# Kernel tuning notes

Measured on AMD Instinct MI355X. Metric: run time of the kernel, lower is better.

## Reference

```python
import jax, jax.numpy as jnp
import numpy as np

B = 1024; PAST = 64; FUT = 16; N = PAST + FUT; DM = N // 3; HID = 64
EMB = [(2000, 32), (7, 8), (24, 8)]
OUTP = 3 + 32 + 8 + 8  # 51 = out_preprocess
O = OUTP - 1           # 50
HID1 = 64; HID2 = 64
NEG = -1e30  # finite stand-in for -inf so fully-masked rows stay NaN-free


def _gcnn(x, A, W, act):
    # D = diag((1 + rowsum(sign(relu(A-1e-15))))^-0.5); out = act(D @ A @ D @ (x W^T))
    d = (1.0 + (A > 1e-15).astype(x.dtype).sum(1)) ** -0.5
    An = d[:, None] * A * d[None, :]            # (P,P)
    h = jnp.einsum('pq,bqc->bpc', An, x @ W.T)  # (B,P,out)
    return jax.nn.relu(h) if act else h


def _forward(data, emb0, emb1, emb2, w1, b1, w2, b2, w3, b3,
             M, Wg1a, Wg1b, Wk, smoothing, Wg2a, Wg2b):
    # learned adjacency: masked softmax over strictly-lower-triangular support
    mask = jnp.tril(jnp.ones((N, N), data.dtype), -1)
    A0 = jax.nn.relu(M @ M.T)
    A = jax.nn.softmax(jnp.where(mask > 0, A0, NEG), axis=1)
    A = jnp.where(mask > 0, A, 0.0)
    # pre_processing: embeddings + MLP, then re-append last raw column
    tabs = (emb0, emb1, emb2)
    e = [t[data[:, :, i].astype(jnp.int32)] for i, t in enumerate(tabs)]
    h = jnp.concatenate(e + [data[:, :, -3:]], -1)        # (B,N,51)
    h = jax.nn.relu(h @ w1.T + b1)
    h = jax.nn.relu(h @ w2.T + b2)
    h = h @ w3.T + b3                                      # (B,N,50)
    x = jnp.concatenate([h, data[:, :, -1:]], -1)          # (B,N,51)
    sg1, sg2 = x[:, :PAST], x[:, PAST:]
    A11 = A[:PAST, :PAST]
    x1 = _gcnn(_gcnn(sg1, A11, Wg1a, True), A11, Wg1b, False)   # (B,PAST,50)
    xk = jnp.concatenate([x1, sg2[:, :, :-1]], 1)               # (B,N,50)
    y = x[:, :PAST, -1:]                                        # (B,PAST,1)
    # Kernel: batched Mahalanobis quadratic form (diagonal computed directly)
    xp, xf = xk[:, :PAST], xk[:, PAST:]
    theta = Wk @ Wk.T
    theta = (theta + theta.T) / 2
    diff = xp[:, None, :, :] - xf[:, :, None, :]                # (B,F,P,50)
    q = jnp.einsum('bjip,pq,bjiq->bji', diff, theta, diff)      # (B,F,P)
    alpha = -0.5 * q / (jax.nn.sigmoid(smoothing[0]) * 0.01)
    At = A[FUT:, :PAST] if False else A[PAST:, :PAST]           # (F,P)
    At = jax.nn.softmax(jnp.where(At != 0, At, NEG), axis=1)
    # torch Softmax(dim=1) on (B,F,P) normalizes over the F axis
    alpha = jax.nn.softmax(jnp.where(At[None] >= 0.004, alpha, NEG), axis=1)
    yh = jnp.einsum('bjp,bpo->bjo', alpha, y)                   # (B,F,1)
    x2 = jnp.concatenate([sg2[:, :, :-1], yh], -1)              # (B,F,51)
    A22 = A[PAST:, PAST:]
    out = _gcnn(_gcnn(x2, A22, Wg2a, True), A22, Wg2b, False).reshape(-1, FUT)
    # cdist(x, x), p=2, with NaN-safe sqrt at zero distance
    xc = jnp.concatenate([sg1, x2], 1)                          # (B,N,51)
    sq = jnp.sum(xc * xc, -1)
    d2 = jnp.maximum(sq[:, :, None] + sq[:, None, :]
                     - 2.0 * jnp.einsum('bnc,bmc->bnm', xc, xc), 0.0)
    dist = jnp.where(d2 > 0, jnp.sqrt(jnp.where(d2 > 0, d2, 1.0)), 0.0)
    return (out, dist, A)


def setup_inputs() -> dict:
    key = jax.random.key(0)
    ks = jax.random.split(key, 20)
    cols = [jax.random.randint(ks[i], (B, N, 1), 0, EMB[i][0]).astype(jnp.float32)
            for i in range(3)]
    data = jnp.concatenate(cols + [jax.random.normal(ks[3], (B, N, 3), jnp.float32)], -1)
    g = lambda k, s, sc: jax.random.normal(k, s, jnp.float32) * sc
    return dict(
        data=data,
        emb0=g(ks[4], EMB[0], 1.0),
        emb1=g(ks[5], EMB[1], 1.0),
        emb2=g(ks[6], EMB[2], 1.0),
        w1=g(ks[7], (128, OUTP), OUTP ** -0.5), b1=jnp.zeros((128,), jnp.float32),
        w2=g(ks[8], (128, 128), 128 ** -0.5), b2=jnp.zeros((128,), jnp.float32),
        w3=g(ks[9], (O, 128), 128 ** -0.5), b3=jnp.zeros((O,), jnp.float32),
        M=g(ks[10], (N, DM), 1.0),
        Wg1a=g(ks[11], (HID1, OUTP), OUTP ** -0.5),
        Wg1b=g(ks[12], (O, HID1), HID1 ** -0.5),
        Wk=g(ks[13], (O, HID), 0.05),
        smoothing=g(ks[14], (1,), 1.0),
        Wg2a=g(ks[15], (HID2, OUTP), OUTP ** -0.5),
        Wg2b=g(ks[16], (1, HID2), HID2 ** -0.5),
    )


def reference(data, emb0, emb1, emb2, w1, b1, w2, b2, w3, b3,
              M, Wg1a, Wg1b, Wk, smoothing, Wg2a, Wg2b):
    return _forward(data, emb0, emb1, emb2, w1, b1, w2, b2, w3, b3,
                    M, Wg1a, Wg1b, Wk, smoothing, Wg2a, Wg2b)
```

## Files before the change

### kernel.cpp

```cpp
#include <hip/hip_runtime.h>
#include <math.h>


#define NEGBIG (-1e30f)

#define OFF_X     0
#define OFF_X1    4177920
#define OFF_YH    7454720
#define OFF_A     7471104
#define OFF_AN22  7481600
#define OFF_MK    7484356
#define OFF_GAH   7514692
#define OFF_GAL   7516740
#define OFF_G2AT  7521156
#define OFF_SC    7524420
#define OFF_W1H   7524424
#define OFF_W1L   7528520
#define OFF_W2H   7532616
#define OFF_W2L   7540808
#define OFF_W3H   7549000
#define OFF_W3L   7553096
#define OFF_ANH   7557192
#define OFF_ANL   7559240
#define OFF_GBH   7561288
#define OFF_GBL   7563336
#define OFF_WKH   7565384
#define OFF_WKL   7567432

#define OUT_OUT   0
#define OUT_DIST  16384
#define OUT_A     6569984

typedef __attribute__((ext_vector_type(8))) short bf16x8;
typedef __attribute__((ext_vector_type(4))) short s16x4;
typedef __attribute__((ext_vector_type(4))) float f32x4;

__device__ __forceinline__ unsigned short f2bf(float x) {
  union { float f; unsigned u; } v; v.f = x;
  unsigned r = v.u + 0x7fffu + ((v.u >> 16) & 1u);
  return (unsigned short)(r >> 16);
}
__device__ __forceinline__ float bf2f(unsigned short h) {
  union { unsigned u; float f; } v; v.u = ((unsigned)h) << 16; return v.f;
}
__device__ __forceinline__ void split2(float v, unsigned short& h, unsigned short& l) {
  unsigned short hh = f2bf(v);
  h = hh;
  l = f2bf(v - bf2f(hh));
}
#define SWZ6(r, k) (((r) << 6) + (((((k) >> 3) ^ ((r) & 7)) << 3) | ((k) & 7)))
#define SWZ7(r, k) (((r) << 7) + (((((k) >> 3) ^ ((r) & 7)) << 3) | ((k) & 7)))

__global__ __launch_bounds__(256) void k_prep(
    const float* __restrict__ M, const float* __restrict__ Wk,
    const float* __restrict__ sm,
    const float* __restrict__ w1, const float* __restrict__ w2,
    const float* __restrict__ w3,
    const float* __restrict__ wg1a, const float* __restrict__ wg1b,
    const float* __restrict__ wg2a,
    float* __restrict__ ws, float* __restrict__ out)
{
  __shared__ float Msh[80 * 26];
  __shared__ float Ash[80 * 80];
  __shared__ float d1[64];
  __shared__ float d2s[16];
  const int t = threadIdx.x;

  if (blockIdx.x == 0) {
    for (int e = t; e < 80 * 26; e += 256) Msh[e] = M[e];
    __syncthreads();
    for (int e = t; e < 6400; e += 256) {
      int i = e / 80, j = e % 80;
      float v = 0.f;
      if (j < i) {
        float s = 0.f;
        for (int k = 0; k < 26; ++k) s += Msh[i * 26 + k] * Msh[j * 26 + k];
        v = s > 0.f ? s : 0.f;
      }
      Ash[e] = v;
    }
    __syncthreads();
    if (t > 0 && t < 80) {
      int i = t;
      float m = -3.4e38f;
      for (int j = 0; j < i; ++j) m = fmaxf(m, Ash[i * 80 + j]);
      float s = 0.f;
      for (int j = 0; j < i; ++j) {
        float e = expf(Ash[i * 80 + j] - m);
        Ash[i * 80 + j] = e;
        s += e;
      }
      float inv = 1.f / s;
      for (int j = 0; j < i; ++j) Ash[i * 80 + j] *= inv;
    }
    __syncthreads();
    {
      float* Aws = ws + OFF_A;
      float* Aout = out + OUT_A;
      for (int e = t; e < 6400; e += 256) { Aws[e] = Ash[e]; Aout[e] = Ash[e]; }
    }
    if (t < 64) {
      int c = 0;
      for (int j = 0; j < 64; ++j) if (Ash[t * 80 + j] > 1e-15f) ++c;
      d1[t] = 1.f / sqrtf(1.f + (float)c);
    } else if (t < 80) {
      int i = t - 64; int c = 0;
      for (int j = 0; j < 16; ++j) if (Ash[(64 + i) * 80 + 64 + j] > 1e-15f) ++c;
      d2s[i] = 1.f / sqrtf(1.f + (float)c);
    }
    __syncthreads();
    {
      float* an22 = ws + OFF_AN22;
      unsigned short* anH = (unsigned short*)(ws + OFF_ANH);
      unsigned short* anL = (unsigned short*)(ws + OFF_ANL);
      for (int e = t; e < 4096; e += 256) {
        int i = e >> 6, j = e & 63;
        float v = d1[i] * Ash[i * 80 + j] * d1[j];
        unsigned short h = f2bf(v);
        anH[e] = h; anL[e] = f2bf(v - bf2f(h));
      }
      for (int e = t; e < 256; e += 256) {
        int i = e >> 4, j = e & 15;
        an22[e] = d2s[i] * Ash[(64 + i) * 80 + 64 + j] * d2s[j];
      }
    }
    if (t < 16) {
      float* mk = ws + OFF_MK;
      int j = t;
      float m = -3.4e38f;
      for (int i = 0; i < 64; ++i) {
        float v = Ash[(64 + j) * 80 + i];
        v = (v != 0.f) ? v : NEGBIG;
        m = fmaxf(m, v);
      }
      float s = 0.f;
      for (int i = 0; i < 64; ++i) {
        float v = Ash[(64 + j) * 80 + i];
        v = (v != 0.f) ? v : NEGBIG;
        s += expf(v - m);
      }
      float inv = 1.f / s;
      for (int i = 0; i < 64; ++i) {
        float v = Ash[(64 + j) * 80 + i];
        v = (v != 0.f) ? v : NEGBIG;
        mk[j * 64 + i] = (expf(v - m) * inv >= 0.004f) ? 1.f : 0.f;
      }
    }
  } else if (blockIdx.x == 1) {
    unsigned short* wkh = (unsigned short*)(ws + OFF_WKH);
    unsigned short* wkl = (unsigned short*)(ws + OFF_WKL);
    for (int e = t; e < 4096; e += 256) {
      int h = e >> 6, o = e & 63;
      float v = (o < 50) ? Wk[o * 64 + h] : 0.f;
      unsigned short hh = f2bf(v);
      wkh[e] = hh; wkl[e] = f2bf(v - bf2f(hh));
    }
    if (t == 0) {
      float v = sm[0];
      float sig = 1.f / (1.f + expf(-v));
      (ws + OFF_SC)[0] = -0.5f / (sig * 0.01f);
    }
  } else if (blockIdx.x == 2) {
    unsigned short* w1h = (unsigned short*)(ws + OFF_W1H);
    unsigned short* w1l = (unsigned short*)(ws + OFF_W1L);
    for (int e = t; e < 8192; e += 256) {
      int n = e >> 6, k = e & 63;
      float v = (k < 51) ? w1[n * 51 + k] : 0.f;
      unsigned short h = f2bf(v);
      w1h[e] = h; w1l[e] = f2bf(v - bf2f(h));
    }
    unsigned short* w3h = (unsigned short*)(ws + OFF_W3H);
    unsigned short* w3l = (unsigned short*)(ws + OFF_W3L);
    for (int e = t; e < 8192; e += 256) {
      int n = e >> 7, k = e & 127;
      float v = (n < 50) ? w3[n * 128 + k] : 0.f;
      unsigned short h = f2bf(v);
      w3h[e] = h; w3l[e] = f2bf(v - bf2f(h));
    }
    unsigned short* gah = (unsigned short*)(ws + OFF_GAH);
    unsigned short* gal = (unsigned short*)(ws + OFF_GAL);
    for (int e = t; e < 4096; e += 256) {
      int n = e >> 6, k = e & 63;
      float v = (k < 51) ? wg1a[n * 51 + k] : 0.f;
      unsigned short h = f2bf(v);
      gah[e] = h; gal[e] = f2bf(v - bf2f(h));
    }
  } else {
    unsigned short* w2h = (unsigned short*)(ws + OFF_W2H);
    unsigned short* w2l = (unsigned short*)(ws + OFF_W2L);
    for (int e = t; e < 16384; e += 256) {
      int n = e >> 7, k = e & 127;
      float v = w2[n * 128 + k];
      unsigned short h = f2bf(v);
      w2h[e] = h; w2l[e] = f2bf(v - bf2f(h));
    }
    unsigned short* gbh = (unsigned short*)(ws + OFF_GBH);
    unsigned short* gbl = (unsigned short*)(ws + OFF_GBL);
    for (int e = t; e < 4096; e += 256) {
      int n = e >> 6, k = e & 63;
      float v = (n < 50) ? wg1b[n * 64 + k] : 0.f;
      unsigned short h = f2bf(v);
      gbh[e] = h; gbl[e] = f2bf(v - bf2f(h));
    }
    float* g2at = ws + OFF_G2AT;
    for (int e = t; e < 64 * 51; e += 256) { int o = e / 51, k = e % 51; g2at[k * 64 + o] = wg2a[e]; }
  }
}

__global__ __launch_bounds__(512) void k_mlp(
    const float* __restrict__ data,
    const float* __restrict__ emb0, const float* __restrict__ emb1,
    const float* __restrict__ emb2,
    const float* __restrict__ b1, const float* __restrict__ b2,
    const float* __restrict__ b3,
    float* __restrict__ ws)
{
  __shared__ __align__(16) unsigned short actH[64 * 128];
  __shared__ __align__(16) unsigned short actL[64 * 128];
  __shared__ __align__(16) unsigned short wbH[8192];
  __shared__ __align__(16) unsigned short wbL[8192];
  const int t = threadIdx.x;
  const int lane = t & 63, wave = t >> 6;
  const int s = wave & 3, half = wave >> 2;
  const int m16 = lane & 15, quad = lane >> 4;
  const int base = blockIdx.x * 64;
  const int row0 = s * 16;
  const int arow = row0 + m16;
  const unsigned short* w1h = (const unsigned short*)(ws + OFF_W1H);
  const unsigned short* w1l = (const unsigned short*)(ws + OFF_W1L);
  const unsigned short* w2h = (const unsigned short*)(ws + OFF_W2H);
  const unsigned short* w2l = (const unsigned short*)(ws + OFF_W2L);
  const unsigned short* w3h = (const unsigned short*)(ws + OFF_W3H);
  const unsigned short* w3l = (const unsigned short*)(ws + OFF_W3L);
  float* x = ws + OFF_X;

  for (int e = t; e < 4096; e += 512) {
    int r = e >> 6, c = e & 63;
    int g = base + r;
    float v = 0.f;
    if (c < 32)      { int i0 = (int)data[g * 6 + 0]; v = emb0[i0 * 32 + c]; }
    else if (c < 40) { int i1 = (int)data[g * 6 + 1]; v = emb1[i1 * 8 + (c - 32)]; }
    else if (c < 48) { int i2 = (int)data[g * 6 + 2]; v = emb2[i2 * 8 + (c - 40)]; }
    else if (c < 51) { v = data[g * 6 + 3 + (c - 48)]; }
    int idx = SWZ7(r, c);
    split2(v, actH[idx], actL[idx]);
  }
  for (int q = t; q < 1024; q += 512) {
    int col = q >> 3, c = q & 7;
    int dst = (col << 6) + ((c ^ (col & 7)) << 3);
    *(bf16x8*)(wbH + dst) = *(const bf16x8*)(w1h + (col << 6) + (c << 3));
    *(bf16x8*)(wbL + dst) = *(const bf16x8*)(w1l + (col << 6) + (c << 3));
  }
  __syncthreads();

  {
    f32x4 acc[4];
#pragma unroll
    for (int n = 0; n < 4; ++n) acc[n] = (f32x4){0.f, 0.f, 0.f, 0.f};
#pragma unroll
    for (int kb8 = 0; kb8 < 8; kb8 += 4) {
      int ach = ((quad + kb8) ^ (m16 & 7)) << 3;
      bf16x8 aH = *(const bf16x8*)(actH + (arow << 7) + ach);
      bf16x8 aL = *(const bf16x8*)(actL + (arow << 7) + ach);
#pragma unroll
      for (int n = 0; n < 4; ++n) {
        const int col = (half * 4 + n) * 16 + m16;
        int boff = (col << 6) + ach;
        bf16x8 bH = *(const bf16x8*)(wbH + boff);
        bf16x8 bL = *(const bf16x8*)(wbL + boff);
        acc[n] = __builtin_amdgcn_mfma_f32_16x16x32_bf16(aH, bH, acc[n], 0, 0, 0);
        acc[n] = __builtin_amdgcn_mfma_f32_16x16x32_bf16(aH, bL, acc[n], 0, 0, 0);
        acc[n] = __builtin_amdgcn_mfma_f32_16x16x32_bf16(aL, bH, acc[n], 0, 0, 0);
      }
    }
#pragma unroll
    for (int n = 0; n < 4; ++n) {
      const int col = (half * 4 + n) * 16 + m16;
      const float bias = b1[col];
#pragma unroll
      for (int r = 0; r < 4; ++r) {
        float v = acc[n][r] + bias; v = v > 0.f ? v : 0.f;
        int idx = SWZ7(row0 + quad * 4 + r, col);
        split2(v, actH[idx], actL[idx]);
      }
    }
  }

  f32x4 acc2[2][2];
#pragma unroll
  for (int a2 = 0; a2 < 2; ++a2)
#pragma unroll
    for (int n = 0; n < 2; ++n) acc2[a2][n] = (f32x4){0.f, 0.f, 0.f, 0.f};
  for (int h2 = 0; h2 < 2; ++h2) {
    __syncthreads();
    for (int q = t; q < 1024; q += 512) {
      int coll = q >> 4, c = q & 15;
      int srcc = (((h2 << 6) + coll) << 7) + (c << 3);
      int dst = (coll << 7) + ((c ^ (coll & 7)) << 3);
      *(bf16x8*)(wbH + dst) = *(const bf16x8*)(w2h + srcc);
      *(bf16x8*)(wbL + dst) = *(const bf16x8*)(w2l + srcc);
    }
    __syncthreads();
#pragma unroll
    for (int kb8 = 0; kb8 < 16; kb8 += 4) {
      int ach = ((quad + kb8) ^ (m16 & 7)) << 3;
      bf16x8 aH = *(const bf16x8*)(actH + (arow << 7) + ach);
      bf16x8 aL = *(const bf16x8*)(actL + (arow << 7) + ach);
#pragma unroll
      for (int n = 0; n < 2; ++n) {
        const int cl = (half * 2 + n) * 16 + m16;
        int boff = (cl << 7) + ach;
        bf16x8 bH = *(const bf16x8*)(wbH + boff);
        bf16x8 bL = *(const bf16x8*)(wbL + boff);
        f32x4 a = acc2[h2][n];
        a = __builtin_amdgcn_mfma_f32_16x16x32_bf16(aH, bH, a, 0, 0, 0);
        a = __builtin_amdgcn_mfma_f32_16x16x32_bf16(aH, bL, a, 0, 0, 0);
        a = __builtin_amdgcn_mfma_f32_16x16x32_bf16(aL, bH, a, 0, 0, 0);
        acc2[h2][n] = a;
      }
    }
  }
  __syncthreads();
#pragma unroll
  for (int hh = 0; hh < 2; ++hh) {
#pragma unroll
    for (int n = 0; n < 2; ++n) {
      const int col = hh * 64 + (half * 2 + n) * 16 + m16;
      const float bias = b2[col];
#pragma unroll
      for (int r = 0; r < 4; ++r) {
        float v = acc2[hh][n][r] + bias; v = v > 0.f ? v : 0.f;
        int idx = SWZ7(row0 + quad * 4 + r, col);
        split2(v, actH[idx], actL[idx]);
      }
    }
  }

  for (int q = t; q < 1024; q += 512) {
    int coll = q >> 4, c = q & 15;
    int dst = (coll << 7) + ((c ^ (coll & 7)) << 3);
    *(bf16x8*)(wbH + dst) = *(const bf16x8*)(w3h + (coll << 7) + (c << 3));
    *(bf16x8*)(wbL + dst) = *(const bf16x8*)(w3l + (coll << 7) + (c << 3));
  }
  __syncthreads();
  {
    f32x4 acc[2];
#pragma unroll
    for (int n = 0; n < 2; ++n) acc[n] = (f32x4){0.f, 0.f, 0.f, 0.f};
#pragma unroll
    for (int kb8 = 0; kb8 < 16; kb8 += 4) {
      int ach = ((quad + kb8) ^ (m16 & 7)) << 3;
      bf16x8 aH = *(const bf16x8*)(actH + (arow << 7) + ach);
      bf16x8 aL = *(const bf16x8*)(actL + (arow << 7) + ach);
#pragma unroll
      for (int n = 0; n < 2; ++n) {
        const int col = (half * 2 + n) * 16 + m16;
        int boff = (col << 7) + ach;
        bf16x8 bH = *(const bf16x8*)(wbH + boff);
        bf16x8 bL = *(const bf16x8*)(wbL + boff);
        acc[n] = __builtin_amdgcn_mfma_f32_16x16x32_bf16(aH, bH, acc[n], 0, 0, 0);
        acc[n] = __builtin_amdgcn_mfma_f32_16x16x32_bf16(aH, bL, acc[n], 0, 0, 0);
        acc[n] = __builtin_amdgcn_mfma_f32_16x16x32_bf16(aL, bH, acc[n], 0, 0, 0);
      }
    }
#pragma unroll
    for (int n = 0; n < 2; ++n) {
      const int col = (half * 2 + n) * 16 + m16;
      if (col < 50) {
        const float bias = b3[col];
#pragma unroll
        for (int r = 0; r < 4; ++r) {
          int row = row0 + quad * 4 + r;
          x[(base + row) * 51 + col] = acc[n][r] + bias;
        }
      }
    }
  }
  if (t < 64) x[(base + t) * 51 + 50] = data[(base + t) * 6 + 5];
}

__global__ __launch_bounds__(512) void k_g1(float* __restrict__ ws)
{
  __shared__ __align__(16) unsigned short b1H[4096], b1L[4096];
  __shared__ __align__(16) unsigned short b2H[4096], b2L[4096];
  __shared__ __align__(16) unsigned short anH[4096], anL[4096];
  __shared__ __align__(16) unsigned short wH[4096],  wL[4096];
  const int t = threadIdx.x, b = blockIdx.x;
  const int lane = t & 63, wave = t >> 6;
  const int s = wave & 3, half = wave >> 2;
  const int m16 = lane & 15, quad = lane >> 4;
  const int row0 = s * 16;
  const int arow = row0 + m16;
  const float* x = ws + OFF_X;
  const unsigned short* gAnH = (const unsigned short*)(ws + OFF_ANH);
  const unsigned short* gAnL = (const unsigned short*)(ws + OFF_ANL);
  const unsigned short* gaH = (const unsigned short*)(ws + OFF_GAH);
  const unsigned short* gaL = (const unsigned short*)(ws + OFF_GAL);
  const unsigned short* gbH = (const unsigned short*)(ws + OFF_GBH);
  const unsigned short* gbL = (const unsigned short*)(ws + OFF_GBL);
  float* x1 = ws + OFF_X1;

  for (int e = t; e < 4096; e += 512) {
    int r = e >> 6, k = e & 63;
    float v = (k < 51) ? x[(b * 80 + r) * 51 + k] : 0.f;
    int idx = SWZ6(r, k);
    split2(v, b1H[idx], b1L[idx]);
  }
  for (int q = t; q < 512; q += 512) {
    int r = q >> 3, c = q & 7;
    int dst = (r << 6) + ((c ^ (r & 7)) << 3);
    int src = (r << 6) + (c << 3);
    *(bf16x8*)(anH + dst) = *(const bf16x8*)(gAnH + src);
    *(bf16x8*)(anL + dst) = *(const bf16x8*)(gAnL + src);
    *(bf16x8*)(wH + dst)  = *(const bf16x8*)(gaH + src);
    *(bf16x8*)(wL + dst)  = *(const bf16x8*)(gaL + src);
  }
  __syncthreads();

  {
    f32x4 acc[2];
#pragma unroll
    for (int n = 0; n < 2; ++n) acc[n] = (f32x4){0.f, 0.f, 0.f, 0.f};
#pragma unroll
    for (int kb8 = 0; kb8 < 8; kb8 += 4) {
      int ach = ((quad + kb8) ^ (m16 & 7)) << 3;
      bf16x8 aH = *(const bf16x8*)(b1H + (arow << 6) + ach);
      bf16x8 aL = *(const bf16x8*)(b1L + (arow << 6) + ach);
#pragma unroll
      for (int n = 0; n < 2; ++n) {
        const int col = (half * 2 + n) * 16 + m16;
        int boff = (col << 6) + ach;
        bf16x8 bH = *(const bf16x8*)(wH + boff);
        bf16x8 bL = *(const bf16x8*)(wL + boff);
        acc[n] = __builtin_amdgcn_mfma_f32_16x16x32_bf16(aH, bH, acc[n], 0, 0, 0);
        acc[n] = __builtin_amdgcn_mfma_f32_16x16x32_bf16(aH, bL, acc[n], 0, 0, 0);
        acc[n] = __builtin_amdgcn_mfma_f32_16x16x32_bf16(aL, bH, acc[n], 0, 0, 0);
      }
    }
    const int kb = row0 + quad * 4;
#pragma unroll
    for (int n = 0; n < 2; ++n) {
      const int col = (half * 2 + n) * 16 + m16;
      int idx = (col << 6) + (((((kb >> 3) ^ (col & 7)) << 3)) | (kb & 7));
      s16x4 hv, lv;
#pragma unroll
      for (int r = 0; r < 4; ++r) {
        unsigned short hh, ll; split2(acc[n][r], hh, ll);
        hv[r] = (short)hh; lv[r] = (short)ll;
      }
      *(s16x4*)(b2H + idx) = hv; *(s16x4*)(b2L + idx) = lv;
    }
  }
  __syncthreads();

  for (int q = t; q < 512; q += 512) {
    int r = q >> 3, c = q & 7;
    int dst = (r << 6) + ((c ^ (r & 7)) << 3);
    int src = (r << 6) + (c << 3);
    *(bf16x8*)(wH + dst) = *(const bf16x8*)(gbH + src);
    *(bf16x8*)(wL + dst) = *(const bf16x8*)(gbL + src);
  }
  f32x4 accP[2];
  {
#pragma unroll
    for (int n = 0; n < 2; ++n) accP[n] = (f32x4){0.f, 0.f, 0.f, 0.f};
#pragma unroll
    for (int kb8 = 0; kb8 < 8; kb8 += 4) {
      int ach = ((quad + kb8) ^ (m16 & 7)) << 3;
      bf16x8 aH = *(const bf16x8*)(anH + (arow << 6) + ach);
      bf16x8 aL = *(const bf16x8*)(anL + (arow << 6) + ach);
#pragma unroll
      for (int n = 0; n < 2; ++n) {
        const int col = (half * 2 + n) * 16 + m16;
        int boff = (col << 6) + ach;
        bf16x8 bH = *(const bf16x8*)(b2H + boff);
        bf16x8 bL = *(const bf16x8*)(b2L + boff);
        accP[n] = __builtin_amdgcn_mfma_f32_16x16x32_bf16(aH, bH, accP[n], 0, 0, 0);
        accP[n] = __builtin_amdgcn_mfma_f32_16x16x32_bf16(aH, bL, accP[n], 0, 0, 0);
        accP[n] = __builtin_amdgcn_mfma_f32_16x16x32_bf16(aL, bH, accP[n], 0, 0, 0);
      }
    }
  }
  __syncthreads();
  {
    const int kb = row0 + quad * 4;
#pragma unroll
    for (int n = 0; n < 2; ++n) {
      const int col = (half * 2 + n) * 16 + m16;
      int idx = (col << 6) + (((((kb >> 3) ^ (col & 7)) << 3)) | (kb & 7));
      s16x4 hv, lv;
#pragma unroll
      for (int r = 0; r < 4; ++r) {
        float v = accP[n][r]; v = v > 0.f ? v : 0.f;
        unsigned short hh, ll; split2(v, hh, ll);
        hv[r] = (short)hh; lv[r] = (short)ll;
      }
      *(s16x4*)(b2H + idx) = hv; *(s16x4*)(b2L + idx) = lv;
    }
  }
  __syncthreads();

  {
    f32x4 acc[2];
#pragma unroll
    for (int n = 0; n < 2; ++n) acc[n] = (f32x4){0.f, 0.f, 0.f, 0.f};
#pragma unroll
    for (int kb8 = 0; kb8 < 8; kb8 += 4) {
      int ach = ((quad + kb8) ^ (m16 & 7)) << 3;
      bf16x8 aH = *(const bf16x8*)(anH + (arow << 6) + ach);
      bf16x8 aL = *(const bf16x8*)(anL + (arow << 6) + ach);
#pragma unroll
      for (int n = 0; n < 2; ++n) {
        const int col = (half * 2 + n) * 16 + m16;
        int boff = (col << 6) + ach;
        bf16x8 bH = *(const bf16x8*)(b2H + boff);
        bf16x8 bL = *(const bf16x8*)(b2L + boff);
        acc[n] = __builtin_amdgcn_mfma_f32_16x16x32_bf16(aH, bH, acc[n], 0, 0, 0);
        acc[n] = __builtin_amdgcn_mfma_f32_16x16x32_bf16(aH, bL, acc[n], 0, 0, 0);
        acc[n] = __builtin_amdgcn_mfma_f32_16x16x32_bf16(aL, bH, acc[n], 0, 0, 0);
      }
    }
#pragma unroll
    for (int n = 0; n < 2; ++n) {
      const int col = (half * 2 + n) * 16 + m16;
#pragma unroll
      for (int r = 0; r < 4; ++r) {
        int idx = SWZ6(row0 + quad * 4 + r, col);
        split2(acc[n][r], b1H[idx], b1L[idx]);
      }
    }
  }
  __syncthreads();

  {
    f32x4 acc[2];
#pragma unroll
    for (int n = 0; n < 2; ++n) acc[n] = (f32x4){0.f, 0.f, 0.f, 0.f};
#pragma unroll
    for (int kb8 = 0; kb8 < 8; kb8 += 4) {
      int ach = ((quad + kb8) ^ (m16 & 7)) << 3;
      bf16x8 aH = *(const bf16x8*)(b1H + (arow << 6) + ach);
      bf16x8 aL = *(const bf16x8*)(b1L + (arow << 6) + ach);
#pragma unroll
      for (int n = 0; n < 2; ++n) {
        const int col = (half * 2 + n) * 16 + m16;
        int boff = (col << 6) + ach;
        bf16x8 bH = *(const bf16x8*)(wH + boff);
        bf16x8 bL = *(const bf16x8*)(wL + boff);
        acc[n] = __builtin_amdgcn_mfma_f32_16x16x32_bf16(aH, bH, acc[n], 0, 0, 0);
        acc[n] = __builtin_amdgcn_mfma_f32_16x16x32_bf16(aH, bL, acc[n], 0, 0, 0);
        acc[n] = __builtin_amdgcn_mfma_f32_16x16x32_bf16(aL, bH, acc[n], 0, 0, 0);
      }
    }
#pragma unroll
    for (int n = 0; n < 2; ++n) {
      const int col = (half * 2 + n) * 16 + m16;
      if (col < 50) {
#pragma unroll
        for (int r = 0; r < 4; ++r) {
          int row = row0 + quad * 4 + r;
          x1[(b * 64 + row) * 50 + col] = acc[n][r];
        }
      }
    }
  }
}

__global__ __launch_bounds__(512) void k_q(const float* __restrict__ wg2b,
                                           float* __restrict__ ws,
                                           float* __restrict__ out)
{
  __shared__ __align__(16) unsigned short zH[4096], zL[4096];
  __shared__ __align__(16) unsigned char bufB[16384];
  __shared__ __align__(16) unsigned short xfH[1024], xfL[1024];
  __shared__ __align__(16) unsigned short zfH[1024], zfL[1024];
  __shared__ float spal[64 * 34];
  __shared__ float sp[64], sf[16], yv[64], yhs[16];
  const int t = threadIdx.x, b = blockIdx.x;
  const int lane = t & 63, wave = t >> 6;
  const int s = wave & 3, half = wave >> 2;
  const int m16 = lane & 15, quad = lane >> 4;
  const int row0 = s * 16;
  const int arow = row0 + m16;
  const float* x = ws + OFF_X;
  const float* x1 = ws + OFF_X1;
  const float* mk = ws + OFF_MK;
  const float* an22 = ws + OFF_AN22;
  const float* g2at = ws + OFF_G2AT;
  const float sc = (ws + OFF_SC)[0];
  float* yh = ws + OFF_YH;

  unsigned short* wkH = (unsigned short*)bufB;
  unsigned short* wkL = wkH + 4096;

  for (int e = t; e < 4096; e += 512) {
    int r = e >> 6, c = e & 63;
    float v = (c < 50) ? x1[(b * 64 + r) * 50 + c] : 0.f;
    int idx = SWZ6(r, c);
    split2(v, zH[idx], zL[idx]);
  }
  for (int e = t; e < 1024; e += 512) {
    int r = e >> 6, c = e & 63;
    float v = (c < 50) ? x[(b * 80 + 64 + r) * 51 + c] : 0.f;
    int idx = SWZ6(r, c);
    split2(v, xfH[idx], xfL[idx]);
  }
  {
    const unsigned short* gwkH = (const unsigned short*)(ws + OFF_WKH);
    const unsigned short* gwkL = (const unsigned short*)(ws + OFF_WKL);
    for (int q = t; q < 512; q += 512) {
      int r = q >> 3, c = q & 7;
      int dst = (r << 6) + ((c ^ (r & 7)) << 3);
      int src = (r << 6) + (c << 3);
      *(bf16x8*)(wkH + dst) = *(const bf16x8*)(gwkH + src);
      *(bf16x8*)(wkL + dst) = *(const bf16x8*)(gwkL + src);
    }
  }
  if (t < 64) yv[t] = x[(b * 80 + t) * 51 + 50];
  __syncthreads();

  f32x4 accZ[2];
#pragma unroll
  for (int n = 0; n < 2; ++n) accZ[n] = (f32x4){0.f, 0.f, 0.f, 0.f};
#pragma unroll
  for (int kb8 = 0; kb8 < 8; kb8 += 4) {
    int ach = ((quad + kb8) ^ (m16 & 7)) << 3;
    bf16x8 aH = *(const bf16x8*)(zH + (arow << 6) + ach);
    bf16x8 aL = *(const bf16x8*)(zL + (arow << 6) + ach);
#pragma unroll
    for (int n = 0; n < 2; ++n) {
      const int col = (half * 2 + n) * 16 + m16;
      int boff = (col << 6) + ach;
      bf16x8 bH = *(const bf16x8*)(wkH + boff);
      bf16x8 bL = *(const bf16x8*)(wkL + boff);
      accZ[n] = __builtin_amdgcn_mfma_f32_16x16x32_bf16(aH, bH, accZ[n], 0, 0, 0);
      accZ[n] = __builtin_amdgcn_mfma_f32_16x16x32_bf16(aH, bL, accZ[n], 0, 0, 0);
      accZ[n] = __builtin_amdgcn_mfma_f32_16x16x32_bf16(aL, bH, accZ[n], 0, 0, 0);
      accZ[n] = __builtin_amdgcn_mfma_f32_16x16x32_bf16(aL, bL, accZ[n], 0, 0, 0);
    }
  }
  if (half == 0) {
    f32x4 af = (f32x4){0.f, 0.f, 0.f, 0.f};
#pragma unroll
    for (int kb8 = 0; kb8 < 8; kb8 += 4) {
      int ach = ((quad + kb8) ^ (m16 & 7)) << 3;
      bf16x8 aH = *(const bf16x8*)(xfH + (m16 << 6) + ach);
      bf16x8 aL = *(const bf16x8*)(xfL + (m16 << 6) + ach);
      const int col = s * 16 + m16;
      int boff = (col << 6) + ach;
      bf16x8 bH = *(const bf16x8*)(wkH + boff);
      bf16x8 bL = *(const bf16x8*)(wkL + boff);
      af = __builtin_amdgcn_mfma_f32_16x16x32_bf16(aH, bH, af, 0, 0, 0);
      af = __builtin_amdgcn_mfma_f32_16x16x32_bf16(aH, bL, af, 0, 0, 0);
      af = __builtin_amdgcn_mfma_f32_16x16x32_bf16(aL, bH, af, 0, 0, 0);
      af = __builtin_amdgcn_mfma_f32_16x16x32_bf16(aL, bL, af, 0, 0, 0);
    }
    const int h = s * 16 + m16;
#pragma unroll
    for (int r = 0; r < 4; ++r) {
      int idx = SWZ6(quad * 4 + r, h);
      split2(af[r], zfH[idx], zfL[idx]);
    }
  }
  __syncthreads();

  {
    float s2[4] = {0.f, 0.f, 0.f, 0.f};
#pragma unroll
    for (int n = 0; n < 2; ++n) {
      const int h = (half * 2 + n) * 16 + m16;
#pragma unroll
      for (int r = 0; r < 4; ++r) {
        float v = accZ[n][r];
        s2[r] += v * v;
        int idx = SWZ6(row0 + quad * 4 + r, h);
        split2(v, zH[idx], zL[idx]);
      }
    }
#pragma unroll
    for (int r = 0; r < 4; ++r)
      spal[(row0 + quad * 4 + r) * 34 + half * 16 + m16] = s2[r];
  }
  __syncthreads();

  if (t < 64) {
    float ssum = 0.f;
#pragma unroll
    for (int m = 0; m < 32; ++m) ssum += spal[t * 34 + m];
    sp[t] = ssum;
  } else if (t < 80) {
    int j = t - 64;
    float ssum = 0.f;
    for (int h = 0; h < 64; ++h) {
      int idx = SWZ6(j, h);
      float v = bf2f(zfH[idx]) + bf2f(zfL[idx]);
      ssum += v * v;
    }
    sf[j] = ssum;
  }
  __syncthreads();

  {
    f32x4 ac2 = (f32x4){0.f, 0.f, 0.f, 0.f};
#pragma unroll
    for (int kb8 = 0; kb8 < 8; kb8 += 4) {
      int ach = ((quad + kb8) ^ (m16 & 7)) << 3;
      bf16x8 aH = *(const bf16x8*)(zH + (arow << 6) + ach);
      bf16x8 aL = *(const bf16x8*)(zL + (arow << 6) + ach);
      bf16x8 bH = *(const bf16x8*)(zfH + (m16 << 6) + ach);
      bf16x8 bL = *(const bf16x8*)(zfL + (m16 << 6) + ach);
      ac2 = __builtin_amdgcn_mfma_f32_16x16x32_bf16(aH, bH, ac2, 0, 0, 0);
      ac2 = __builtin_amdgcn_mfma_f32_16x16x32_bf16(aH, bL, ac2, 0, 0, 0);
      ac2 = __builtin_amdgcn_mfma_f32_16x16x32_bf16(aL, bH, ac2, 0, 0, 0);
      ac2 = __builtin_amdgcn_mfma_f32_16x16x32_bf16(aL, bL, ac2, 0, 0, 0);
    }
    if (half == 0) {
      float* al = spal;
#pragma unroll
      for (int r = 0; r < 4; ++r) {
        int i = row0 + quad * 4 + r;
        al[i * 17 + m16] = sc * (sp[i] + sf[m16] - 2.f * ac2[r]);
      }
    }
  }
  __syncthreads();
  {
    float* al = spal;
    if (t < 64) {
      const int i = t;
      float lv[16];
      float m = -3.4e38f;
#pragma unroll
      for (int j = 0; j < 16; ++j) {
        float v = (mk[j * 64 + i] != 0.f) ? al[i * 17 + j] : NEGBIG;
        lv[j] = v;
        m = fmaxf(m, v);
      }
      float ssum = 0.f;
#pragma unroll
      for (int j = 0; j < 16; ++j) { lv[j] = expf(lv[j] - m); ssum += lv[j]; }
      float inv = 1.f / ssum;
#pragma unroll
      for (int j = 0; j < 16; ++j) al[i * 17 + j] = lv[j] * inv;
    }
  }
  __syncthreads();
  if (t < 16) {
    float* al = spal;
    float ssum = 0.f;
    for (int i = 0; i < 64; ++i) ssum += al[i * 17 + t] * yv[i];
    yh[b * 16 + t] = ssum;
    yhs[t] = ssum;
  }
  __syncthreads();

  float* X2  = (float*)bufB;
  float* A22 = X2 + 832;
  float* G   = A22 + 256;
  float* Pm  = G + 1024;
  float* wb  = Pm + 1024;
  float* zz  = wb + 64;

  for (int e = t; e < 832; e += 512) {
    int r = e / 52, c = e - r * 52;
    float v = 0.f;
    if (c < 50)       v = x[(b * 80 + 64 + r) * 51 + c];
    else if (c == 50) v = yhs[r];
    X2[e] = v;
  }
  for (int e = t; e < 256; e += 512) A22[e] = an22[e];
  if (t < 64) wb[t] = wg2b[t];
  __syncthreads();
  for (int e = t; e < 1024; e += 512) {
    int j = e >> 6, h = e & 63;
    float ssum = 0.f;
    for (int k = 0; k < 51; ++k) ssum += X2[j * 52 + k] * g2at[k * 64 + h];
    G[e] = ssum;
  }
  __syncthreads();
  for (int e = t; e < 1024; e += 512) {
    int j = e >> 6, h = e & 63;
    float ssum = 0.f;
#pragma unroll
    for (int k = 0; k < 16; ++k) ssum += A22[j * 16 + k] * G[k * 64 + h];
    Pm[e] = ssum > 0.f ? ssum : 0.f;
  }
  __syncthreads();
  if (t < 16) {
    float ssum = 0.f;
    for (int h = 0; h < 64; ++h) ssum += Pm[t * 64 + h] * wb[h];
    zz[t] = ssum;
  }
  __syncthreads();
  if (t < 16) {
    float ssum = 0.f;
#pragma unroll
    for (int k = 0; k < 16; ++k) ssum += A22[t * 16 + k] * zz[k];
    out[OUT_OUT + b * 16 + t] = ssum;
  }
}

__global__ __launch_bounds__(320) void k_dist(float* __restrict__ ws,
                                              float* __restrict__ out)
{
  __shared__ __align__(16) unsigned short xcH[5120], xcL[5120];
  __shared__ float sq[80];
  const int t = threadIdx.x, b = blockIdx.x;
  const int lane = t & 63, wave = t >> 6;
  const int m16 = lane & 15, quad = lane >> 4;
  const int row0 = wave * 16;
  const int arow = row0 + m16;
  const float* x = ws + OFF_X;
  const float* yhg = ws + OFF_YH;
  float* dist = out + OUT_DIST + b * 6400;

  for (int e = t; e < 5120; e += 320) {
    int n = e >> 6, c = e & 63;
    float v = 0.f;
    if (c < 50)       v = x[(b * 80 + n) * 51 + c];
    else if (c == 50) v = (n < 64) ? x[(b * 80 + n) * 51 + 50] : yhg[b * 16 + (n - 64)];
    int idx = SWZ6(n, c);
    split2(v, xcH[idx], xcL[idx]);
  }
  __syncthreads();

  f32x4 acc[5];
#pragma unroll
  for (int n = 0; n < 5; ++n) acc[n] = (f32x4){0.f, 0.f, 0.f, 0.f};
#pragma unroll
  for (int kb8 = 0; kb8 < 8; kb8 += 4) {
    int ach = ((quad + kb8) ^ (m16 & 7)) << 3;
    bf16x8 aH = *(const bf16x8*)(xcH + (arow << 6) + ach);
    bf16x8 aL = *(const bf16x8*)(xcL + (arow << 6) + ach);
#pragma unroll
    for (int nf = 0; nf < 5; ++nf) {
      const int col = nf * 16 + m16;
      int boff = (col << 6) + ach;
      bf16x8 bH = *(const bf16x8*)(xcH + boff);
      bf16x8 bL = *(const bf16x8*)(xcL + boff);
      acc[nf] = __builtin_amdgcn_mfma_f32_16x16x32_bf16(aH, bH, acc[nf], 0, 0, 0);
      acc[nf] = __builtin_amdgcn_mfma_f32_16x16x32_bf16(aH, bL, acc[nf], 0, 0, 0);
      acc[nf] = __builtin_amdgcn_mfma_f32_16x16x32_bf16(aL, bH, acc[nf], 0, 0, 0);
    }
  }
  if ((m16 >> 2) == quad) sq[row0 + m16] = acc[wave][m16 & 3];
  __syncthreads();

#pragma unroll
  for (int nf = 0; nf < 5; ++nf) {
    const int m = nf * 16 + m16;
#pragma unroll
    for (int r = 0; r < 4; ++r) {
      int i = row0 + quad * 4 + r;
      float d2 = sq[i] + sq[m] - 2.f * acc[nf][r];
      d2 = d2 > 0.f ? d2 : 0.f;
      dist[i * 80 + m] = d2 > 0.f ? sqrtf(d2) : 0.f;
    }
  }
}

extern "C" void kernel_launch(void* const* d_in, const int* in_sizes, int n_in,
                              void* d_out, int out_size, void* d_ws, size_t ws_size,
                              hipStream_t stream)
{
  const float* data = (const float*)d_in[0];
  const float* emb0 = (const float*)d_in[1];
  const float* emb1 = (const float*)d_in[2];
  const float* emb2 = (const float*)d_in[3];
  const float* w1   = (const float*)d_in[4];
  const float* b1   = (const float*)d_in[5];
  const float* w2   = (const float*)d_in[6];
  const float* b2   = (const float*)d_in[7];
  const float* w3   = (const float*)d_in[8];
  const float* b3   = (const float*)d_in[9];
  const float* M    = (const float*)d_in[10];
  const float* wg1a = (const float*)d_in[11];
  const float* wg1b = (const float*)d_in[12];
  const float* Wk   = (const float*)d_in[13];
  const float* smo  = (const float*)d_in[14];
  const float* wg2a = (const float*)d_in[15];
  const float* wg2b = (const float*)d_in[16];
  float* ws  = (float*)d_ws;
  float* out = (float*)d_out;

  k_prep<<<dim3(4),    dim3(256), 0, stream>>>(M, Wk, smo, w1, w2, w3, wg1a, wg1b, wg2a, ws, out);
  k_mlp <<<dim3(1280), dim3(512), 0, stream>>>(data, emb0, emb1, emb2, b1, b2, b3, ws);
  k_g1  <<<dim3(1024), dim3(512), 0, stream>>>(ws);
  k_q   <<<dim3(1024), dim3(512), 0, stream>>>(wg2b, ws, out);
  k_dist<<<dim3(1024), dim3(320), 0, stream>>>(ws, out);
}
```

Baseline: 228.6 us.

## Fuse GCN and kernel-attention stages into one kernel; prefetch MLP weights

Merges the k_g1 and k_q kernels into a single k_gq kernel, so the GCN output x1 stays in shared memory and is never written to or re-read from global memory. This also removes one launch. Shared memory is reused across phases through aliasing. The row-norm reduction now uses wave shuffles instead of a shared-memory sum. In k_mlp, the next layer's weights are loaded into registers while the current MFMA runs, which hides global latency but raises register pressure.

Result: faster. 213.6 us (-6.6%).

```diff
diff --git a/kernel.cpp b/kernel.cpp
--- a/kernel.cpp
+++ b/kernel.cpp
@@ -5,7 +5,6 @@
 #define NEGBIG (-1e30f)
 
 #define OFF_X     0
-#define OFF_X1    4177920
 #define OFF_YH    7454720
 #define OFF_A     7471104
 #define OFF_AN22  7481600
@@ -50,6 +49,14 @@
 }
 #define SWZ6(r, k) (((r) << 6) + (((((k) >> 3) ^ ((r) & 7)) << 3) | ((k) & 7)))
 #define SWZ7(r, k) (((r) << 7) + (((((k) >> 3) ^ ((r) & 7)) << 3) | ((k) & 7)))
+
+#define MFMA3(acc, aH, aL, bH, bL) \
+  acc = __builtin_amdgcn_mfma_f32_16x16x32_bf16(aH, bH, acc, 0, 0, 0); \
+  acc = __builtin_amdgcn_mfma_f32_16x16x32_bf16(aH, bL, acc, 0, 0, 0); \
+  acc = __builtin_amdgcn_mfma_f32_16x16x32_bf16(aL, bH, acc, 0, 0, 0);
+#define MFMA4(acc, aH, aL, bH, bL) \
+  MFMA3(acc, aH, aL, bH, bL) \
+  acc = __builtin_amdgcn_mfma_f32_16x16x32_bf16(aL, bL, acc, 0, 0, 0);
 
 __global__ __launch_bounds__(256) void k_prep(
     const float* __restrict__ M, const float* __restrict__ Wk,
@@ -251,6 +258,16 @@
     *(bf16x8*)(wbH + dst) = *(const bf16x8*)(w1h + (col << 6) + (c << 3));
     *(bf16x8*)(wbL + dst) = *(const bf16x8*)(w1l + (col << 6) + (c << 3));
   }
+  bf16x8 pH[2], pL[2];
+#pragma unroll
+  for (int i = 0; i < 2; ++i) {
+    int q = t + i * 512;
+    int coll = q >> 4, c = q & 15;
+    int src = (coll << 7) + (c << 3);
+    pH[i] = *(const bf16x8*)(w2h + src);
+    pL[i] = *(const bf16x8*)(w2l + src);
+  }
+  if (t < 64) x[(base + t) * 51 + 50] = data[(base + t) * 6 + 5];
   __syncthreads();
 
   {
@@ -268,9 +285,7 @@
         int boff = (col << 6) + ach;
         bf16x8 bH = *(const bf16x8*)(wbH + boff);
         bf16x8 bL = *(const bf16x8*)(wbL + boff);
-        acc[n] = __builtin_amdgcn_mfma_f32_16x16x32_bf16(aH, bH, acc[n], 0, 0, 0);
-        acc[n] = __builtin_amdgcn_mfma_f32_16x16x32_bf16(aH, bL, acc[n], 0, 0, 0);
-        acc[n] = __builtin_amdgcn_mfma_f32_16x16x32_bf16(aL, bH, acc[n], 0, 0, 0);
+        MFMA3(acc[n], aH, aL, bH, bL)
       }
     }
 #pragma unroll
@@ -285,42 +300,81 @@
       }
     }
   }
+  __syncthreads();
+
+#pragma unroll
+  for (int i = 0; i < 2; ++i) {
+    int q = t + i * 512;
+    int coll = q >> 4, c = q & 15;
+    int dst = (coll << 7) + ((c ^ (coll & 7)) << 3);
+    *(bf16x8*)(wbH + dst) = pH[i];
+    *(bf16x8*)(wbL + dst) = pL[i];
+  }
+#pragma unroll
+  for (int i = 0; i < 2; ++i) {
+    int q = t + i * 512;
+    int coll = q >> 4, c = q & 15;
+    int src = ((64 + coll) << 7) + (c << 3);
+    pH[i] = *(const bf16x8*)(w2h + src);
+    pL[i] = *(const bf16x8*)(w2l + src);
+  }
+  __syncthreads();
 
   f32x4 acc2[2][2];
 #pragma unroll
   for (int a2 = 0; a2 < 2; ++a2)
 #pragma unroll
     for (int n = 0; n < 2; ++n) acc2[a2][n] = (f32x4){0.f, 0.f, 0.f, 0.f};
-  for (int h2 = 0; h2 < 2; ++h2) {
-    __syncthreads();
-    for (int q = t; q < 1024; q += 512) {
-      int coll = q >> 4, c = q & 15;
-      int srcc = (((h2 << 6) + coll) << 7) + (c << 3);
-      int dst = (coll << 7) + ((c ^ (coll & 7)) << 3);
-      *(bf16x8*)(wbH + dst) = *(const bf16x8*)(w2h + srcc);
-      *(bf16x8*)(wbL + dst) = *(const bf16x8*)(w2l + srcc);
-    }
-    __syncthreads();
-#pragma unroll
-    for (int kb8 = 0; kb8 < 16; kb8 += 4) {
-      int ach = ((quad + kb8) ^ (m16 & 7)) << 3;
-      bf16x8 aH = *(const bf16x8*)(actH + (arow << 7) + ach);
-      bf16x8 aL = *(const bf16x8*)(actL + (arow << 7) + ach);
-#pragma unroll
-      for (int n = 0; n < 2; ++n) {
-        const int cl = (half * 2 + n) * 16 + m16;
-        int boff = (cl << 7) + ach;
-        bf16x8 bH = *(const bf16x8*)(wbH + boff);
-        bf16x8 bL = *(const bf16x8*)(wbL + boff);
-        f32x4 a = acc2[h2][n];
-        a = __builtin_amdgcn_mfma_f32_16x16x32_bf16(aH, bH, a, 0, 0, 0);
-        a = __builtin_amdgcn_mfma_f32_16x16x32_bf16(aH, bL, a, 0, 0, 0);
-        a = __builtin_amdgcn_mfma_f32_16x16x32_bf16(aL, bH, a, 0, 0, 0);
-        acc2[h2][n] = a;
-      }
-    }
-  }
-  __syncthreads();
+#pragma unroll
+  for (int kb8 = 0; kb8 < 16; kb8 += 4) {
+    int ach = ((quad + kb8) ^ (m16 & 7)) << 3;
+    bf16x8 aH = *(const bf16x8*)(actH + (arow << 7) + ach);
+    bf16x8 aL = *(const bf16x8*)(actL + (arow << 7) + ach);
+#pragma unroll
+    for (int n = 0; n < 2; ++n) {
+      const int cl = (half * 2 + n) * 16 + m16;
+      int boff = (cl << 7) + ach;
+      bf16x8 bH = *(const bf16x8*)(wbH + boff);
+      bf16x8 bL = *(const bf16x8*)(wbL + boff);
+      MFMA3(acc2[0][n], aH, aL, bH, bL)
+    }
+  }
+  __syncthreads();
+
+#pragma unroll
+  for (int i = 0; i < 2; ++i) {
+    int q = t + i * 512;
+    int coll = q >> 4, c = q & 15;
+    int dst = (coll << 7) + ((c ^ (coll & 7)) << 3);
+    *(bf16x8*)(wbH + dst) = pH[i];
+    *(bf16x8*)(wbL + dst) = pL[i];
+  }
+#pragma unroll
+  for (int i = 0; i < 2; ++i) {
+    int q = t + i * 512;
+    int coll = q >> 4, c = q & 15;
+    int src = (coll << 7) + (c << 3);
+    pH[i] = *(const bf16x8*)(w3h + src);
+    pL[i] = *(const bf16x8*)(w3l + src);
+  }
+  __syncthreads();
+
+#pragma unroll
+  for (int kb8 = 0; kb8 < 16; kb8 += 4) {
+    int ach = ((quad + kb8) ^ (m16 & 7)) << 3;
+    bf16x8 aH = *(const bf16x8*)(actH + (arow << 7) + ach);
+    bf16x8 aL = *(const bf16x8*)(actL + (arow << 7) + ach);
+#pragma unroll
+    for (int n = 0; n < 2; ++n) {
+      const int cl = (half * 2 + n) * 16 + m16;
+      int boff = (cl << 7) + ach;
+      bf16x8 bH = *(const bf16x8*)(wbH + boff);
+      bf16x8 bL = *(const bf16x8*)(wbL + boff);
+      MFMA3(acc2[1][n], aH, aL, bH, bL)
+    }
+  }
+  __syncthreads();
+
 #pragma unroll
   for (int hh = 0; hh < 2; ++hh) {
 #pragma unroll
@@ -335,14 +389,16 @@
       }
     }
   }
-
-  for (int q = t; q < 1024; q += 512) {
+#pragma unroll
+  for (int i = 0; i < 2; ++i) {
+    int q = t + i * 512;
     int coll = q >> 4, c = q & 15;
     int dst = (coll << 7) + ((c ^ (coll & 7)) << 3);
-    *(bf16x8*)(wbH + dst) = *(const bf16x8*)(w3h + (coll << 7) + (c << 3));
-    *(bf16x8*)(wbL + dst) = *(const bf16x8*)(w3l + (coll << 7) + (c << 3));
-  }
-  __syncthreads();
+    *(bf16x8*)(wbH + dst) = pH[i];
+    *(bf16x8*)(wbL + dst) = pL[i];
+  }
+  __syncthreads();
+
   {
     f32x4 acc[2];
 #pragma unroll
@@ -358,9 +414,7 @@
         int boff = (col << 7) + ach;
         bf16x8 bH = *(const bf16x8*)(wbH + boff);
         bf16x8 bL = *(const bf16x8*)(wbL + boff);
-        acc[n] = __builtin_amdgcn_mfma_f32_16x16x32_bf16(aH, bH, acc[n], 0, 0, 0);
-        acc[n] = __builtin_amdgcn_mfma_f32_16x16x32_bf16(aH, bL, acc[n], 0, 0, 0);
-        acc[n] = __builtin_amdgcn_mfma_f32_16x16x32_bf16(aL, bH, acc[n], 0, 0, 0);
+        MFMA3(acc[n], aH, aL, bH, bL)
       }
     }
 #pragma unroll
@@ -376,15 +430,38 @@
       }
     }
   }
-  if (t < 64) x[(base + t) * 51 + 50] = data[(base + t) * 6 + 5];
 }
 
-__global__ __launch_bounds__(512) void k_g1(float* __restrict__ ws)
+__global__ __launch_bounds__(512) void k_gq(const float* __restrict__ wg2b,
+                                            float* __restrict__ ws,
+                                            float* __restrict__ out)
 {
-  __shared__ __align__(16) unsigned short b1H[4096], b1L[4096];
-  __shared__ __align__(16) unsigned short b2H[4096], b2L[4096];
-  __shared__ __align__(16) unsigned short anH[4096], anL[4096];
-  __shared__ __align__(16) unsigned short wH[4096],  wL[4096];
+  __shared__ __align__(16) unsigned short SH[32768];
+  unsigned short* b1H = SH;
+  unsigned short* b1L = SH + 4096;
+  unsigned short* b2H = SH + 8192;
+  unsigned short* b2L = SH + 12288;
+  unsigned short* anH = SH + 16384;
+  unsigned short* anL = SH + 20480;
+  unsigned short* wH  = SH + 24576;
+  unsigned short* wL  = SH + 28672;
+  unsigned short* xfH = SH + 24576;
+  unsigned short* xfL = SH + 25600;
+  unsigned short* zfH = SH + 26624;
+  unsigned short* zfL = SH + 27648;
+  float* alS  = (float*)(SH + 28672);
+  float* spH2 = (float*)(SH + 30848);
+  float* spS  = (float*)(SH + 31104);
+  float* sfS  = (float*)(SH + 31232);
+  float* yvS  = (float*)(SH + 31264);
+  float* yhsS = (float*)(SH + 31392);
+  float* X2v  = (float*)(SH + 8192);
+  float* A22v = X2v + 832;
+  float* G2v  = A22v + 256;
+  float* Pmv  = G2v + 1024;
+  float* wb2  = Pmv + 1024;
+  float* zzv  = wb2 + 64;
+
   const int t = threadIdx.x, b = blockIdx.x;
   const int lane = t & 63, wave = t >> 6;
   const int s = wave & 3, half = wave >> 2;
@@ -392,13 +469,19 @@
   const int row0 = s * 16;
   const int arow = row0 + m16;
   const float* x = ws + OFF_X;
+  const float* mk = ws + OFF_MK;
+  const float* an22 = ws + OFF_AN22;
+  const float* g2at = ws + OFF_G2AT;
   const unsigned short* gAnH = (const unsigned short*)(ws + OFF_ANH);
   const unsigned short* gAnL = (const unsigned short*)(ws + OFF_ANL);
   const unsigned short* gaH = (const unsigned short*)(ws + OFF_GAH);
   const unsigned short* gaL = (const unsigned short*)(ws + OFF_GAL);
   const unsigned short* gbH = (const unsigned short*)(ws + OFF_GBH);
   const unsigned short* gbL = (const unsigned short*)(ws + OFF_GBL);
-  float* x1 = ws + OFF_X1;
+  const unsigned short* gwkH = (const unsigned short*)(ws + OFF_WKH);
+  const unsigned short* gwkL = (const unsigned short*)(ws + OFF_WKL);
+  const float sc = (ws + OFF_SC)[0];
+  float* yh = ws + OFF_YH;
 
   for (int e = t; e < 4096; e += 512) {
     int r = e >> 6, k = e & 63;
@@ -406,37 +489,50 @@
     int idx = SWZ6(r, k);
     split2(v, b1H[idx], b1L[idx]);
   }
-  for (int q = t; q < 512; q += 512) {
+  {
+    int q = t;
+    if (q < 512) {
+      int r = q >> 3, c = q & 7;
+      int dst = (r << 6) + ((c ^ (r & 7)) << 3);
+      int src = (r << 6) + (c << 3);
+      *(bf16x8*)(anH + dst) = *(const bf16x8*)(gAnH + src);
+      *(bf16x8*)(anL + dst) = *(const bf16x8*)(gAnL + src);
+      *(bf16x8*)(wH + dst)  = *(const bf16x8*)(gaH + src);
+      *(bf16x8*)(wL + dst)  = *(const bf16x8*)(gaL + src);
+    }
+  }
+  float yvreg = 0.f;
+  if (t < 64) yvreg = x[(b * 80 + t) * 51 + 50];
+  bf16x8 pH, pL;
+  {
+    int q = t & 511;
     int r = q >> 3, c = q & 7;
-    int dst = (r << 6) + ((c ^ (r & 7)) << 3);
     int src = (r << 6) + (c << 3);
-    *(bf16x8*)(anH + dst) = *(const bf16x8*)(gAnH + src);
-    *(bf16x8*)(anL + dst) = *(const bf16x8*)(gAnL + src);
-    *(bf16x8*)(wH + dst)  = *(const bf16x8*)(gaH + src);
-    *(bf16x8*)(wL + dst)  = *(const bf16x8*)(gaL + src);
-  }
-  __syncthreads();
-
-  {
-    f32x4 acc[2];
-#pragma unroll
-    for (int n = 0; n < 2; ++n) acc[n] = (f32x4){0.f, 0.f, 0.f, 0.f};
-#pragma unroll
-    for (int kb8 = 0; kb8 < 8; kb8 += 4) {
-      int ach = ((quad + kb8) ^ (m16 & 7)) << 3;
-      bf16x8 aH = *(const bf16x8*)(b1H + (arow << 6) + ach);
-      bf16x8 aL = *(const bf16x8*)(b1L + (arow << 6) + ach);
-#pragma unroll
-      for (int n = 0; n < 2; ++n) {
-        const int col = (half * 2 + n) * 16 + m16;
-        int boff = (col << 6) + ach;
-        bf16x8 bH = *(const bf16x8*)(wH + boff);
-        bf16x8 bL = *(const bf16x8*)(wL + boff);
-        acc[n] = __builtin_amdgcn_mfma_f32_16x16x32_bf16(aH, bH, acc[n], 0, 0, 0);
-        acc[n] = __builtin_amdgcn_mfma_f32_16x16x32_bf16(aH, bL, acc[n], 0, 0, 0);
-        acc[n] = __builtin_amdgcn_mfma_f32_16x16x32_bf16(aL, bH, acc[n], 0, 0, 0);
-      }
-    }
+    pH = *(const bf16x8*)(gbH + src);
+    pL = *(const bf16x8*)(gbL + src);
+  }
+  __syncthreads();
+
+  f32x4 accA[2];
+#pragma unroll
+  for (int n = 0; n < 2; ++n) accA[n] = (f32x4){0.f, 0.f, 0.f, 0.f};
+#pragma unroll
+  for (int kb8 = 0; kb8 < 8; kb8 += 4) {
+    int ach = ((quad + kb8) ^ (m16 & 7)) << 3;
+    bf16x8 aH = *(const bf16x8*)(b1H + (arow << 6) + ach);
+    bf16x8 aL = *(const bf16x8*)(b1L + (arow << 6) + ach);
+#pragma unroll
+    for (int n = 0; n < 2; ++n) {
+      const int col = (half * 2 + n) * 16 + m16;
+      int boff = (col << 6) + ach;
+      bf16x8 bH = *(const bf16x8*)(wH + boff);
+      bf16x8 bL = *(const bf16x8*)(wL + boff);
+      MFMA3(accA[n], aH, aL, bH, bL)
+    }
+  }
+  __syncthreads();
+
+  {
     const int kb = row0 + quad * 4;
 #pragma unroll
     for (int n = 0; n < 2; ++n) {
@@ -445,43 +541,42 @@
       s16x4 hv, lv;
 #pragma unroll
       for (int r = 0; r < 4; ++r) {
-        unsigned short hh, ll; split2(acc[n][r], hh, ll);
+        unsigned short hh, ll; split2(accA[n][r], hh, ll);
         hv[r] = (short)hh; lv[r] = (short)ll;
       }
       *(s16x4*)(b2H + idx) = hv; *(s16x4*)(b2L + idx) = lv;
     }
   }
-  __syncthreads();
-
-  for (int q = t; q < 512; q += 512) {
+  {
+    int q = t & 511;
     int r = q >> 3, c = q & 7;
     int dst = (r << 6) + ((c ^ (r & 7)) << 3);
+    *(bf16x8*)(wH + dst) = pH;
+    *(bf16x8*)(wL + dst) = pL;
     int src = (r << 6) + (c << 3);
-    *(bf16x8*)(wH + dst) = *(const bf16x8*)(gbH + src);
-    *(bf16x8*)(wL + dst) = *(const bf16x8*)(gbL + src);
-  }
-  f32x4 accP[2];
-  {
-#pragma unroll
-    for (int n = 0; n < 2; ++n) accP[n] = (f32x4){0.f, 0.f, 0.f, 0.f};
-#pragma unroll
-    for (int kb8 = 0; kb8 < 8; kb8 += 4) {
-      int ach = ((quad + kb8) ^ (m16 & 7)) << 3;
-      bf16x8 aH = *(const bf16x8*)(anH + (arow << 6) + ach);
-      bf16x8 aL = *(const bf16x8*)(anL + (arow << 6) + ach);
-#pragma unroll
-      for (int n = 0; n < 2; ++n) {
-        const int col = (half * 2 + n) * 16 + m16;
-        int boff = (col << 6) + ach;
-        bf16x8 bH = *(const bf16x8*)(b2H + boff);
-        bf16x8 bL = *(const bf16x8*)(b2L + boff);
-        accP[n] = __builtin_amdgcn_mfma_f32_16x16x32_bf16(aH, bH, accP[n], 0, 0, 0);
-        accP[n] = __builtin_amdgcn_mfma_f32_16x16x32_bf16(aH, bL, accP[n], 0, 0, 0);
-        accP[n] = __builtin_amdgcn_mfma_f32_16x16x32_bf16(aL, bH, accP[n], 0, 0, 0);
-      }
-    }
-  }
-  __syncthreads();
+    pH = *(const bf16x8*)(gwkH + src);
+    pL = *(const bf16x8*)(gwkL + src);
+  }
+  __syncthreads();
+
+#pragma unroll
+  for (int n = 0; n < 2; ++n) accA[n] = (f32x4){0.f, 0.f, 0.f, 0.f};
+#pragma unroll
+  for (int kb8 = 0; kb8 < 8; kb8 += 4) {
+    int ach = ((quad + kb8) ^ (m16 & 7)) << 3;
+    bf16x8 aH = *(const bf16x8*)(anH + (arow << 6) + ach);
+    bf16x8 aL = *(const bf16x8*)(anL + (arow << 6) + ach);
+#pragma unroll
+    for (int n = 0; n < 2; ++n) {
+      const int col = (half * 2 + n) * 16 + m16;
+      int boff = (col << 6) + ach;
+      bf16x8 bH = *(const bf16x8*)(b2H + boff);
+      bf16x8 bL = *(const bf16x8*)(b2L + boff);
+      MFMA3(accA[n], aH, aL, bH, bL)
+    }
+  }
+  __syncthreads();
+
   {
     const int kb = row0 + quad * 4;
 #pragma unroll
@@ -491,7 +586,7 @@
       s16x4 hv, lv;
 #pragma unroll
       for (int r = 0; r < 4; ++r) {
-        float v = accP[n][r]; v = v > 0.f ? v : 0.f;
+        float v = accA[n][r]; v = v > 0.f ? v : 0.f;
         unsigned short hh, ll; split2(v, hh, ll);
         hv[r] = (short)hh; lv[r] = (short)ll;
       }
@@ -500,143 +595,101 @@
   }
   __syncthreads();
 
-  {
-    f32x4 acc[2];
-#pragma unroll
-    for (int n = 0; n < 2; ++n) acc[n] = (f32x4){0.f, 0.f, 0.f, 0.f};
-#pragma unroll
-    for (int kb8 = 0; kb8 < 8; kb8 += 4) {
-      int ach = ((quad + kb8) ^ (m16 & 7)) << 3;
-      bf16x8 aH = *(const bf16x8*)(anH + (arow << 6) + ach);
-      bf16x8 aL = *(const bf16x8*)(anL + (arow << 6) + ach);
-#pragma unroll
-      for (int n = 0; n < 2; ++n) {
-        const int col = (half * 2 + n) * 16 + m16;
-        int boff = (col << 6) + ach;
-        bf16x8 bH = *(const bf16x8*)(b2H + boff);
-        bf16x8 bL = *(const bf16x8*)(b2L + boff);
-        acc[n] = __builtin_amdgcn_mfma_f32_16x16x32_bf16(aH, bH, acc[n], 0, 0, 0);
-        acc[n] = __builtin_amdgcn_mfma_f32_16x16x32_bf16(aH, bL, acc[n], 0, 0, 0);
-        acc[n] = __builtin_amdgcn_mfma_f32_16x16x32_bf16(aL, bH, acc[n], 0, 0, 0);
-      }
-    }
-#pragma unroll
-    for (int n = 0; n < 2; ++n) {
-      const int col = (half * 2 + n) * 16 + m16;
-#pragma unroll
-      for (int r = 0; r < 4; ++r) {
-        int idx = SWZ6(row0 + quad * 4 + r, col);
-        split2(acc[n][r], b1H[idx], b1L[idx]);
-      }
-    }
-  }
-  __syncthreads();
-
-  {
-    f32x4 acc[2];
-#pragma unroll
-    for (int n = 0; n < 2; ++n) acc[n] = (f32x4){0.f, 0.f, 0.f, 0.f};
-#pragma unroll
-    for (int kb8 = 0; kb8 < 8; kb8 += 4) {
-      int ach = ((quad + kb8) ^ (m16 & 7)) << 3;
-      bf16x8 aH = *(const bf16x8*)(b1H + (arow << 6) + ach);
-      bf16x8 aL = *(const bf16x8*)(b1L + (arow << 6) + ach);
-#pragma unroll
-      for (int n = 0; n < 2; ++n) {
-        const int col = (half * 2 + n) * 16 + m16;
-        int boff = (col << 6) + ach;
-        bf16x8 bH = *(const bf16x8*)(wH + boff);
-        bf16x8 bL = *(const bf16x8*)(wL + boff);
-        acc[n] = __builtin_amdgcn_mfma_f32_16x16x32_bf16(aH, bH, acc[n], 0, 0, 0);
-        acc[n] = __builtin_amdgcn_mfma_f32_16x16x32_bf16(aH, bL, acc[n], 0, 0, 0);
-        acc[n] = __builtin_amdgcn_mfma_f32_16x16x32_bf16(aL, bH, acc[n], 0, 0, 0);
-      }
-    }
-#pragma unroll
-    for (int n = 0; n < 2; ++n) {
-      const int col = (half * 2 + n) * 16 + m16;
-      if (col < 50) {
-#pragma unroll
-        for (int r = 0; r < 4; ++r) {
-          int row = row0 + quad * 4 + r;
-          x1[(b * 64 + row) * 50 + col] = acc[n][r];
-        }
-      }
-    }
-  }
-}
-
-__global__ __launch_bounds__(512) void k_q(const float* __restrict__ wg2b,
-                                           float* __restrict__ ws,
-                                           float* __restrict__ out)
-{
-  __shared__ __align__(16) unsigned short zH[4096], zL[4096];
-  __shared__ __align__(16) unsigned char bufB[16384];
-  __shared__ __align__(16) unsigned short xfH[1024], xfL[1024];
-  __shared__ __align__(16) unsigned short zfH[1024], zfL[1024];
-  __shared__ float spal[64 * 34];
-  __shared__ float sp[64], sf[16], yv[64], yhs[16];
-  const int t = threadIdx.x, b = blockIdx.x;
-  const int lane = t & 63, wave = t >> 6;
-  const int s = wave & 3, half = wave >> 2;
-  const int m16 = lane & 15, quad = lane >> 4;
-  const int row0 = s * 16;
-  const int arow = row0 + m16;
-  const float* x = ws + OFF_X;
-  const float* x1 = ws + OFF_X1;
-  const float* mk = ws + OFF_MK;
-  const float* an22 = ws + OFF_AN22;
-  const float* g2at = ws + OFF_G2AT;
-  const float sc = (ws + OFF_SC)[0];
-  float* yh = ws + OFF_YH;
-
-  unsigned short* wkH = (unsigned short*)bufB;
-  unsigned short* wkL = wkH + 4096;
-
-  for (int e = t; e < 4096; e += 512) {
-    int r = e >> 6, c = e & 63;
-    float v = (c < 50) ? x1[(b * 64 + r) * 50 + c] : 0.f;
-    int idx = SWZ6(r, c);
-    split2(v, zH[idx], zL[idx]);
-  }
-  for (int e = t; e < 1024; e += 512) {
-    int r = e >> 6, c = e & 63;
-    float v = (c < 50) ? x[(b * 80 + 64 + r) * 51 + c] : 0.f;
-    int idx = SWZ6(r, c);
-    split2(v, xfH[idx], xfL[idx]);
-  }
-  {
-    const unsigned short* gwkH = (const unsigned short*)(ws + OFF_WKH);
-    const unsigned short* gwkL = (const unsigned short*)(ws + OFF_WKL);
-    for (int q = t; q < 512; q += 512) {
-      int r = q >> 3, c = q & 7;
-      int dst = (r << 6) + ((c ^ (r & 7)) << 3);
-      int src = (r << 6) + (c << 3);
-      *(bf16x8*)(wkH + dst) = *(const bf16x8*)(gwkH + src);
-      *(bf16x8*)(wkL + dst) = *(const bf16x8*)(gwkL + src);
-    }
-  }
-  if (t < 64) yv[t] = x[(b * 80 + t) * 51 + 50];
-  __syncthreads();
-
-  f32x4 accZ[2];
-#pragma unroll
-  for (int n = 0; n < 2; ++n) accZ[n] = (f32x4){0.f, 0.f, 0.f, 0.f};
+#pragma unroll
+  for (int n = 0; n < 2; ++n) accA[n] = (f32x4){0.f, 0.f, 0.f, 0.f};
 #pragma unroll
   for (int kb8 = 0; kb8 < 8; kb8 += 4) {
     int ach = ((quad + kb8) ^ (m16 & 7)) << 3;
-    bf16x8 aH = *(const bf16x8*)(zH + (arow << 6) + ach);
-    bf16x8 aL = *(const bf16x8*)(zL + (arow << 6) + ach);
+    bf16x8 aH = *(const bf16x8*)(anH + (arow << 6) + ach);
+    bf16x8 aL = *(const bf16x8*)(anL + (arow << 6) + ach);
 #pragma unroll
     for (int n = 0; n < 2; ++n) {
       const int col = (half * 2 + n) * 16 + m16;
       int boff = (col << 6) + ach;
-      bf16x8 bH = *(const bf16x8*)(wkH + boff);
-      bf16x8 bL = *(const bf16x8*)(wkL + boff);
-      accZ[n] = __builtin_amdgcn_mfma_f32_16x16x32_bf16(aH, bH, accZ[n], 0, 0, 0);
-      accZ[n] = __builtin_amdgcn_mfma_f32_16x16x32_bf16(aH, bL, accZ[n], 0, 0, 0);
-      accZ[n] = __builtin_amdgcn_mfma_f32_16x16x32_bf16(aL, bH, accZ[n], 0, 0, 0);
-      accZ[n] = __builtin_amdgcn_mfma_f32_16x16x32_bf16(aL, bL, accZ[n], 0, 0, 0);
+      bf16x8 bH = *(const bf16x8*)(b2H + boff);
+      bf16x8 bL = *(const bf16x8*)(b2L + boff);
+      MFMA3(accA[n], aH, aL, bH, bL)
+    }
+  }
+  __syncthreads();
+
+#pragma unroll
+  for (int n = 0; n < 2; ++n) {
+    const int col = (half * 2 + n) * 16 + m16;
+#pragma unroll
+    for (int r = 0; r < 4; ++r) {
+      int idx = SWZ6(row0 + quad * 4 + r, col);
+      split2(accA[n][r], b1H[idx], b1L[idx]);
+    }
+  }
+  {
+    int q = t & 511;
+    int r = q >> 3, c = q & 7;
+    int dst = (r << 6) + ((c ^ (r & 7)) << 3);
+    *(bf16x8*)(anH + dst) = pH;
+    *(bf16x8*)(anL + dst) = pL;
+  }
+  float xf0 = 0.f, xf1 = 0.f;
+  {
+    int e0 = t, e1 = t + 512;
+    int r0r = e0 >> 6, c0 = e0 & 63;
+    int r1r = e1 >> 6, c1 = e1 & 63;
+    if (c0 < 50) xf0 = x[(b * 80 + 64 + r0r) * 51 + c0];
+    if (c1 < 50) xf1 = x[(b * 80 + 64 + r1r) * 51 + c1];
+  }
+  __syncthreads();
+
+#pragma unroll
+  for (int n = 0; n < 2; ++n) accA[n] = (f32x4){0.f, 0.f, 0.f, 0.f};
+#pragma unroll
+  for (int kb8 = 0; kb8 < 8; kb8 += 4) {
+    int ach = ((quad + kb8) ^ (m16 & 7)) << 3;
+    bf16x8 aH = *(const bf16x8*)(b1H + (arow << 6) + ach);
+    bf16x8 aL = *(const bf16x8*)(b1L + (arow << 6) + ach);
+#pragma unroll
+    for (int n = 0; n < 2; ++n) {
+      const int col = (half * 2 + n) * 16 + m16;
+      int boff = (col << 6) + ach;
+      bf16x8 bH = *(const bf16x8*)(wH + boff);
+      bf16x8 bL = *(const bf16x8*)(wL + boff);
+      MFMA3(accA[n], aH, aL, bH, bL)
+    }
+  }
+  __syncthreads();
+
+#pragma unroll
+  for (int n = 0; n < 2; ++n) {
+    const int col = (half * 2 + n) * 16 + m16;
+#pragma unroll
+    for (int r = 0; r < 4; ++r) {
+      int idx = SWZ6(row0 + quad * 4 + r, col);
+      split2(accA[n][r], b2H[idx], b2L[idx]);
+    }
+  }
+  {
+    int e0 = t, e1 = t + 512;
+    int i0 = SWZ6(e0 >> 6, e0 & 63);
+    int i1 = SWZ6(e1 >> 6, e1 & 63);
+    split2(xf0, xfH[i0], xfL[i0]);
+    split2(xf1, xfH[i1], xfL[i1]);
+  }
+  if (t < 64) yvS[t] = yvreg;
+  __syncthreads();
+
+#pragma unroll
+  for (int n = 0; n < 2; ++n) accA[n] = (f32x4){0.f, 0.f, 0.f, 0.f};
+#pragma unroll
+  for (int kb8 = 0; kb8 < 8; kb8 += 4) {
+    int ach = ((quad + kb8) ^ (m16 & 7)) << 3;
+    bf16x8 aH = *(const bf16x8*)(b2H + (arow << 6) + ach);
+    bf16x8 aL = *(const bf16x8*)(b2L + (arow << 6) + ach);
+#pragma unroll
+    for (int n = 0; n < 2; ++n) {
+      const int col = (half * 2 + n) * 16 + m16;
+      int boff = (col << 6) + ach;
+      bf16x8 bH = *(const bf16x8*)(anH + boff);
+      bf16x8 bL = *(const bf16x8*)(anL + boff);
+      MFMA4(accA[n], aH, aL, bH, bL)
     }
   }
   if (half == 0) {
@@ -648,12 +701,9 @@
       bf16x8 aL = *(const bf16x8*)(xfL + (m16 << 6) + ach);
       const int col = s * 16 + m16;
       int boff = (col << 6) + ach;
-      bf16x8 bH = *(const bf16x8*)(wkH + boff);
-      bf16x8 bL = *(const bf16x8*)(wkL + boff);
-      af = __builtin_amdgcn_mfma_f32_16x16x32_bf16(aH, bH, af, 0, 0, 0);
-      af = __builtin_amdgcn_mfma_f32_16x16x32_bf16(aH, bL, af, 0, 0, 0);
-      af = __builtin_amdgcn_mfma_f32_16x16x32_bf16(aL, bH, af, 0, 0, 0);
-      af = __builtin_amdgcn_mfma_f32_16x16x32_bf16(aL, bL, af, 0, 0, 0);
+      bf16x8 bH = *(const bf16x8*)(anH + boff);
+      bf16x8 bL = *(const bf16x8*)(anL + boff);
+      MFMA4(af, aH, aL, bH, bL)
     }
     const int h = s * 16 + m16;
 #pragma unroll
@@ -662,32 +712,34 @@
       split2(af[r], zfH[idx], zfL[idx]);
     }
   }
-  __syncthreads();
-
-  {
-    float s2[4] = {0.f, 0.f, 0.f, 0.f};
+  {
+    float s2[4];
+#pragma unroll
+    for (int r = 0; r < 4; ++r)
+      s2[r] = accA[0][r] * accA[0][r] + accA[1][r] * accA[1][r];
 #pragma unroll
     for (int n = 0; n < 2; ++n) {
       const int h = (half * 2 + n) * 16 + m16;
 #pragma unroll
       for (int r = 0; r < 4; ++r) {
-        float v = accZ[n][r];
-        s2[r] += v * v;
         int idx = SWZ6(row0 + quad * 4 + r, h);
-        split2(v, zH[idx], zL[idx]);
-      }
-    }
-#pragma unroll
-    for (int r = 0; r < 4; ++r)
-      spal[(row0 + quad * 4 + r) * 34 + half * 16 + m16] = s2[r];
+        split2(accA[n][r], b1H[idx], b1L[idx]);
+      }
+    }
+#pragma unroll
+    for (int m = 1; m < 16; m <<= 1)
+#pragma unroll
+      for (int r = 0; r < 4; ++r) s2[r] += __shfl_xor(s2[r], m);
+    if (m16 == 0) {
+#pragma unroll
+      for (int r = 0; r < 4; ++r)
+        spH2[(row0 + quad * 4 + r) * 2 + half] = s2[r];
+    }
   }
   __syncthreads();
 
   if (t < 64) {
-    float ssum = 0.f;
-#pragma unroll
-    for (int m = 0; m < 32; ++m) ssum += spal[t * 34 + m];
-    sp[t] = ssum;
+    spS[t] = spH2[t * 2] + spH2[t * 2 + 1];
   } else if (t < 80) {
     int j = t - 64;
     float ssum = 0.f;
@@ -696,7 +748,7 @@
       float v = bf2f(zfH[idx]) + bf2f(zfL[idx]);
       ssum += v * v;
     }
-    sf[j] = ssum;
+    sfS[j] = ssum;
   }
   __syncthreads();
 
@@ -705,97 +757,84 @@
 #pragma unroll
     for (int kb8 = 0; kb8 < 8; kb8 += 4) {
       int ach = ((quad + kb8) ^ (m16 & 7)) << 3;
-      bf16x8 aH = *(const bf16x8*)(zH + (arow << 6) + ach);
-      bf16x8 aL = *(const bf16x8*)(zL + (arow << 6) + ach);
+      bf16x8 aH = *(const bf16x8*)(b1H + (arow << 6) + ach);
+      bf16x8 aL = *(const bf16x8*)(b1L + (arow << 6) + ach);
       bf16x8 bH = *(const bf16x8*)(zfH + (m16 << 6) + ach);
       bf16x8 bL = *(const bf16x8*)(zfL + (m16 << 6) + ach);
-      ac2 = __builtin_amdgcn_mfma_f32_16x16x32_bf16(aH, bH, ac2, 0, 0, 0);
-      ac2 = __builtin_amdgcn_mfma_f32_16x16x32_bf16(aH, bL, ac2, 0, 0, 0);
-      ac2 = __builtin_amdgcn_mfma_f32_16x16x32_bf16(aL, bH, ac2, 0, 0, 0);
-      ac2 = __builtin_amdgcn_mfma_f32_16x16x32_bf16(aL, bL, ac2, 0, 0, 0);
+      MFMA4(ac2, aH, aL, bH, bL)
     }
     if (half == 0) {
-      float* al = spal;
 #pragma unroll
       for (int r = 0; r < 4; ++r) {
         int i = row0 + quad * 4 + r;
-        al[i * 17 + m16] = sc * (sp[i] + sf[m16] - 2.f * ac2[r]);
-      }
-    }
-  }
-  __syncthreads();
-  {
-    float* al = spal;
-    if (t < 64) {
-      const int i = t;
-      float lv[16];
-      float m = -3.4e38f;
-#pragma unroll
-      for (int j = 0; j < 16; ++j) {
-        float v = (mk[j * 64 + i] != 0.f) ? al[i * 17 + j] : NEGBIG;
-        lv[j] = v;
-        m = fmaxf(m, v);
-      }
-      float ssum = 0.f;
-#pragma unroll
-      for (int j = 0; j < 16; ++j) { lv[j] = expf(lv[j] - m); ssum += lv[j]; }
-      float inv = 1.f / ssum;
-#pragma unroll
-      for (int j = 0; j < 16; ++j) al[i * 17 + j] = lv[j] * inv;
-    }
-  }
-  __syncthreads();
+        alS[i * 17 + m16] = sc * (spS[i] + sfS[m16] - 2.f * ac2[r]);
+      }
+    }
+  }
+  __syncthreads();
+
+  if (t < 64) {
+    const int i = t;
+    float lv[16];
+    float m = -3.4e38f;
+#pragma unroll
+    for (int j = 0; j < 16; ++j) {
+      float v = (mk[j * 64 + i] != 0.f) ? alS[i * 17 + j] : NEGBIG;
+      lv[j] = v;
+      m = fmaxf(m, v);
+    }
+    float ssum = 0.f;
+#pragma unroll
+    for (int j = 0; j < 16; ++j) { lv[j] = expf(lv[j] - m); ssum += lv[j]; }
+    float inv = 1.f / ssum;
+#pragma unroll
+    for (int j = 0; j < 16; ++j) alS[i * 17 + j] = lv[j] * inv;
+  }
+  __syncthreads();
+
   if (t < 16) {
-    float* al = spal;
     float ssum = 0.f;
-    for (int i = 0; i < 64; ++i) ssum += al[i * 17 + t] * yv[i];
+    for (int i = 0; i < 64; ++i) ssum += alS[i * 17 + t] * yvS[i];
     yh[b * 16 + t] = ssum;
-    yhs[t] = ssum;
-  }
-  __syncthreads();
-
-  float* X2  = (float*)bufB;
-  float* A22 = X2 + 832;
-  float* G   = A22 + 256;
-  float* Pm  = G + 1024;
-  float* wb  = Pm + 1024;
-  float* zz  = wb + 64;
+    yhsS[t] = ssum;
+  }
+  __syncthreads();
 
   for (int e = t; e < 832; e += 512) {
     int r = e / 52, c = e - r * 52;
     float v = 0.f;
     if (c < 50)       v = x[(b * 80 + 64 + r) * 51 + c];
-    else if (c == 50) v = yhs[r];
-    X2[e] = v;
-  }
-  for (int e = t; e < 256; e += 512) A22[e] = an22[e];
-  if (t < 64) wb[t] = wg2b[t];
+    else if (c == 50) v = yhsS[r];
+    X2v[e] = v;
+  }
+  for (int e = t; e < 256; e += 512) A22v[e] = an22[e];
+  if (t < 64) wb2[t] = wg2b[t];
   __syncthreads();
   for (int e = t; e < 1024; e += 512) {
     int j = e >> 6, h = e & 63;
     float ssum = 0.f;
-    for (int k = 0; k < 51; ++k) ssum += X2[j * 52 + k] * g2at[k * 64 + h];
-    G[e] = ssum;
+    for (int k = 0; k < 51; ++k) ssum += X2v[j * 52 + k] * g2at[k * 64 + h];
+    G2v[e] = ssum;
   }
   __syncthreads();
   for (int e = t; e < 1024; e += 512) {
     int j = e >> 6, h = e & 63;
     float ssum = 0.f;
 #pragma unroll
-    for (int k = 0; k < 16; ++k) ssum += A22[j * 16 + k] * G[k * 64 + h];
-    Pm[e] = ssum > 0.f ? ssum : 0.f;
+    for (int k = 0; k < 16; ++k) ssum += A22v[j * 16 + k] * G2v[k * 64 + h];
+    Pmv[e] = ssum > 0.f ? ssum : 0.f;
   }
   __syncthreads();
   if (t < 16) {
     float ssum = 0.f;
-    for (int h = 0; h < 64; ++h) ssum += Pm[t * 64 + h] * wb[h];
-    zz[t] = ssum;
+    for (int h = 0; h < 64; ++h) ssum += Pmv[t * 64 + h] * wb2[h];
+    zzv[t] = ssum;
   }
   __syncthreads();
   if (t < 16) {
     float ssum = 0.f;
 #pragma unroll
-    for (int k = 0; k < 16; ++k) ssum += A22[t * 16 + k] * zz[k];
+    for (int k = 0; k < 16; ++k) ssum += A22v[t * 16 + k] * zzv[k];
     out[OUT_OUT + b * 16 + t] = ssum;
   }
 }
@@ -838,9 +877,7 @@
       int boff = (col << 6) + ach;
       bf16x8 bH = *(const bf16x8*)(xcH + boff);
       bf16x8 bL = *(const bf16x8*)(xcL + boff);
-      acc[nf] = __builtin_amdgcn_mfma_f32_16x16x32_bf16(aH, bH, acc[nf], 0, 0, 0);
-      acc[nf] = __builtin_amdgcn_mfma_f32_16x16x32_bf16(aH, bL, acc[nf], 0, 0, 0);
-      acc[nf] = __builtin_amdgcn_mfma_f32_16x16x32_bf16(aL, bH, acc[nf], 0, 0, 0);
+      MFMA3(acc[nf], aH, aL, bH, bL)
     }
   }
   if ((m16 >> 2) == quad) sq[row0 + m16] = acc[wave][m16 & 3];
@@ -885,7 +922,6 @@
 
   k_prep<<<dim3(4),    dim3(256), 0, stream>>>(M, Wk, smo, w1, w2, w3, wg1a, wg1b, wg2a, ws, out);
   k_mlp <<<dim3(1280), dim3(512), 0, stream>>>(data, emb0, emb1, emb2, b1, b2, b3, ws);
-  k_g1  <<<dim3(1024), dim3(512), 0, stream>>>(ws);
-  k_q   <<<dim3(1024), dim3(512), 0, stream>>>(wg2b, ws, out);
+  k_gq  <<<dim3(1024), dim3(512), 0, stream>>>(wg2b, ws, out);
   k_dist<<<dim3(1024), dim3(320), 0, stream>>>(ws, out);
 }
```
